# Performance work log

Measured on AMD Instinct MI355X. Metric: run time of the kernel, lower is better.

Reference implementation:

```python
import jax, jax.numpy as jnp
import numpy as np

T_STEP = 0.01
N_STEPS = 1000
H_S = 64
N_TARGETS = 2048
INPUT_S = 2
H_NN = 256
ACTION_S = 2


def setup_inputs() -> dict:
    key = jax.random.key(0)
    ks = jax.random.split(key, 9)
    target = jax.random.normal(ks[0], (N_TARGETS, INPUT_S), dtype=jnp.float32)
    D = jax.random.normal(ks[1], (H_S,), dtype=jnp.float32) * 0.1
    P = jax.random.normal(ks[2], (H_S, H_S), dtype=jnp.float32)
    l1_w = jax.random.normal(ks[3], (H_NN, INPUT_S), dtype=jnp.float32) * 0.05
    l1_b = jax.random.normal(ks[4], (H_NN,), dtype=jnp.float32) * 0.05
    l2_w = jax.random.normal(ks[5], (H_S, H_NN), dtype=jnp.float32) * 0.05
    l2_b = jax.random.normal(ks[6], (H_S,), dtype=jnp.float32) * 0.05
    lm_w = jax.random.normal(ks[7], (ACTION_S, H_S), dtype=jnp.float32) * 0.05
    lm_b = jax.random.normal(ks[8], (ACTION_S,), dtype=jnp.float32) * 0.05
    return {"target": target, "D": D, "P": P,
            "l1_w": l1_w, "l1_b": l1_b, "l2_w": l2_w, "l2_b": l2_b,
            "lm_w": lm_w, "lm_b": lm_b}


def reference(target, D, P, l1_w, l1_b, l2_w, l2_b, lm_w, lm_b):
    # initial condition MLP: relu(l1) -> l2, then transpose to (h_s, n_targets)
    h = jax.nn.relu(target @ l1_w.T + l1_b)           # (n_targets, h_nn)
    x0 = (h @ l2_w.T + l2_b).T                        # (h_s, n_targets)
    # A = P diag(exp(D)) P^-1 ; step map x <- (I - dt*A) x
    A = (P * jnp.exp(D)[None, :]) @ jnp.linalg.inv(P)  # (h_s, h_s)
    M = jnp.eye(H_S, dtype=A.dtype) - T_STEP * A

    def step(x, _):
        act = jnp.tanh(x.T @ lm_w.T + lm_b)            # (n_targets, action_s)
        return M @ x, (x, act)

    _, (hidden_states, acts) = jax.lax.scan(step, x0, None, length=N_STEPS)
    # hidden_states: (n_steps, h_s, n_targets); acts: (n_steps, n_targets, action_s)
    actions = jnp.transpose(acts, (1, 2, 0))           # (n_targets, action_s, n_steps)
    return actions, hidden_states
```

## Files before the change

### kernel.cpp

```cpp
#include <hip/hip_runtime.h>
#include <math.h>

#define NT 2048
#define HS 64
#define HNN 256
#define NSTEPS 1000
#define TSTEP 0.01f

typedef unsigned short u16;
typedef __attribute__((ext_vector_type(8))) short bf16x8;
typedef __attribute__((ext_vector_type(4))) float f32x4;

#define OFF_PINV 0
#define OFF_HT   148736

#define S_H 1028

__device__ inline void bsplit(float x, u16& hi, u16& lo) {
    unsigned u = __float_as_uint(x);
    unsigned r = (u + 0x7FFFu + ((u >> 16) & 1u)) >> 16;
    hi = (u16)r;
    float xh = __uint_as_float(r << 16);
    float d = x - xh;
    unsigned v = __float_as_uint(d);
    unsigned s = (v + 0x7FFFu + ((v >> 16) & 1u)) >> 16;
    lo = (u16)s;
}

__device__ inline void bar_lds() {
    asm volatile("s_waitcnt lgkmcnt(0)" ::: "memory");
    __builtin_amdgcn_s_barrier();
    asm volatile("" ::: "memory");
}

__device__ inline float tanh_fast(float x) {
    float xc = fminf(fmaxf(x, -15.f), 15.f);
    float a = __builtin_amdgcn_exp2f(xc * 2.885390082f);
    return (a - 1.f) * __builtin_amdgcn_rcpf(a + 1.f);
}

__global__ __launch_bounds__(512) void k_gj(const float* __restrict__ P,
                                            float* __restrict__ ws) {
    __shared__ float Aug[64 * 130];
    __shared__ float fvec[2][64];
    int tid = threadIdx.x;

    for (int idx = tid; idx < 64 * 128; idx += 512) {
        int r = idx >> 7, c = idx & 127;
        Aug[r * 130 + c] = (c < 64) ? P[r * 64 + c] : ((c - 64) == r ? 1.f : 0.f);
    }
    __syncthreads();

    if (tid < 64) {
        float nv = Aug[tid * 130];
        float pv = __shfl(nv, 0);
        fvec[0][tid] = (tid == 0) ? 0.f : nv / pv;
    }
    __syncthreads();

    for (int t = 0; t < 64; ++t) {
        int par = t & 1;
        if (tid < 64) {
            int col0 = (t < 63) ? (t + 1) : 64;
            float f = fvec[par][tid];
            float src = Aug[t * 130 + col0];
            float nv = Aug[tid * 130 + col0] - f * src;
            Aug[tid * 130 + col0] = nv;
            if (t < 63) {
                float pv = __shfl(nv, t + 1);
                fvec[par ^ 1][tid] = (tid == (t + 1)) ? 0.f : nv / pv;
            }
        } else {
            int w = (tid >> 6) - 1;
            int lane = tid & 63;
            float f = fvec[par][lane];
            const float* rowp = Aug + t * 130;
            float* rowr = Aug + lane * 130;
            int pcnt = 63 - t;
            for (int s = 1 + w; s < 64; s += 7) {
                int col = (s < pcnt) ? (t + 1 + s) : (64 + (s - pcnt));
                rowr[col] -= f * rowp[col];
            }
        }
        __syncthreads();
    }

    for (int idx = tid; idx < 4096; idx += 512) {
        int j = idx >> 6, m = idx & 63;
        ws[OFF_PINV + j * 64 + m] = Aug[j * 130 + 64 + m] / Aug[j * 130 + j];
    }
}

__global__ __launch_bounds__(512) void k_y0fa(const float* __restrict__ target,
                                              const float* __restrict__ l1_w,
                                              const float* __restrict__ l1_b,
                                              const float* __restrict__ l2_w,
                                              const float* __restrict__ l2_b,
                                              const float* __restrict__ lm_w,
                                              const float* __restrict__ lm_b,
                                              const float* __restrict__ D,
                                              const float* __restrict__ P,
                                              float* __restrict__ ws,
                                              float* __restrict__ actions) {
    int ct = blockIdx.x;
    int cbase = ct * 16;
    int tid = threadIdx.x;
    __shared__ float tgt[16][2];
    __shared__ union { float shT[256 * 17]; float rs[64 * 17]; float us[16][128]; } u;
    __shared__ float x0s[64 * 17];
    __shared__ float y0s[64 * 17];
    __shared__ float lam_s[64], l2l_s[64];
    __shared__ float Q_s[128];

    if (tid < 16) {
        float2 tv = ((const float2*)target)[cbase + tid];
        tgt[tid][0] = tv.x; tgt[tid][1] = tv.y;
    } else if (tid >= 64 && tid < 128) {
        int i = tid - 64;
        float l = 1.0f - TSTEP * expf(D[i]);
        lam_s[i] = l;
        l2l_s[i] = log2f(l);
    } else if (tid >= 128 && tid < 256) {
        int t = tid - 128;
        int a = t >> 6, i = t & 63;
        float s = 0.f;
        for (int r = 0; r < 64; ++r) s = fmaf(lm_w[a * 64 + r], P[r * 64 + i], s);
        Q_s[t] = s;
    }
    __syncthreads();
    if (tid < 256) {
        float w0 = l1_w[2 * tid], w1 = l1_w[2 * tid + 1], bb = l1_b[tid];
        #pragma unroll
        for (int cc = 0; cc < 16; ++cc)
            u.shT[tid * 17 + cc] =
                fmaxf(fmaf(w0, tgt[cc][0], fmaf(w1, tgt[cc][1], bb)), 0.f);
    }
    __syncthreads();
    int i = tid >> 3, cs = (tid & 7) * 2;
    {
        const float* l2wi = l2_w + i * 256;
        float bb = l2_b[i];
        float a0 = bb, a1 = bb;
        #pragma unroll 4
        for (int j = 0; j < 256; ++j) {
            float w = l2wi[j];
            a0 = fmaf(w, u.shT[j * 17 + cs], a0);
            a1 = fmaf(w, u.shT[j * 17 + cs + 1], a1);
        }
        x0s[i * 17 + cs] = a0; x0s[i * 17 + cs + 1] = a1;
    }
    __syncthreads();
    const float* Ri = ws + OFF_PINV + i * 64;
    {
        float b0 = 0, b1 = 0;
        #pragma unroll 4
        for (int m = 0; m < 64; ++m) {
            float rv = Ri[m];
            b0 = fmaf(rv, x0s[m * 17 + cs], b0);
            b1 = fmaf(rv, x0s[m * 17 + cs + 1], b1);
        }
        y0s[i * 17 + cs] = b0; y0s[i * 17 + cs + 1] = b1;
    }
    __syncthreads();
    const float* Pi = P + i * 64;
    #pragma unroll 1
    for (int it = 0; it < 2; ++it) {
        float r0 = x0s[i * 17 + cs], r1 = x0s[i * 17 + cs + 1];
        #pragma unroll 4
        for (int m = 0; m < 64; ++m) {
            float pv = Pi[m];
            r0 = fmaf(-pv, y0s[m * 17 + cs], r0);
            r1 = fmaf(-pv, y0s[m * 17 + cs + 1], r1);
        }
        u.rs[i * 17 + cs] = r0; u.rs[i * 17 + cs + 1] = r1;
        __syncthreads();
        float d0 = 0, d1 = 0;
        #pragma unroll 4
        for (int m = 0; m < 64; ++m) {
            float rv = Ri[m];
            d0 = fmaf(rv, u.rs[m * 17 + cs], d0);
            d1 = fmaf(rv, u.rs[m * 17 + cs + 1], d1);
        }
        y0s[i * 17 + cs] += d0; y0s[i * 17 + cs + 1] += d1;
        __syncthreads();
    }

    for (int idx = tid; idx < 2048; idx += 512) {
        int cgi = idx >> 7, t = idx & 127;
        u.us[cgi][t] = Q_s[t] * y0s[(t & 63) * 17 + cgi];
    }
    if (tid < 128) {
        int kt = tid >> 6, lane = tid & 63;
        int c_l = lane & 15;
        int i0 = kt * 32 + (lane >> 4) * 8;
        u16* YH = (u16*)(ws + OFF_HT);
        u16* YL = YH + 131072;
        bf16x8 vh, vl;
        #pragma unroll
        for (int j = 0; j < 8; ++j) {
            u16 h, lo;
            bsplit(y0s[(i0 + j) * 17 + c_l], h, lo);
            vh[j] = (short)h; vl[j] = (short)lo;
        }
        int off = ((ct * 2 + kt) * 64 + lane);
        *(bf16x8*)(YH + off * 8) = vh;
        *(bf16x8*)(YL + off * 8) = vl;
    }
    __syncthreads();

    if (tid < 500) {
        int k0 = tid * 2;
        float b0 = lm_b[0], b1 = lm_b[1];
        float fk0 = (float)k0;
        #pragma unroll 1
        for (int ch = 0; ch < 4; ++ch) {
            int cg0 = ch * 4;
            float2 s[4][2];
            #pragma unroll
            for (int j = 0; j < 4; ++j) {
                s[j][0] = make_float2(b0, b0);
                s[j][1] = make_float2(b1, b1);
            }
            #pragma unroll 4
            for (int ii = 0; ii < 64; ++ii) {
                float p0 = __builtin_amdgcn_exp2f(fk0 * l2l_s[ii]);
                float p1 = p0 * lam_s[ii];
                #pragma unroll
                for (int j = 0; j < 4; ++j) {
                    float u0 = u.us[cg0 + j][ii];
                    float u1 = u.us[cg0 + j][64 + ii];
                    s[j][0].x = fmaf(u0, p0, s[j][0].x);
                    s[j][0].y = fmaf(u0, p1, s[j][0].y);
                    s[j][1].x = fmaf(u1, p0, s[j][1].x);
                    s[j][1].y = fmaf(u1, p1, s[j][1].y);
                }
            }
            #pragma unroll
            for (int j = 0; j < 4; ++j)
                #pragma unroll
                for (int a = 0; a < 2; ++a) {
                    float2 r;
                    r.x = tanh_fast(s[j][a].x);
                    r.y = tanh_fast(s[j][a].y);
                    *(float2*)(actions + (size_t)(cbase + cg0 + j) * 2000 + a * 1000 + k0) = r;
                }
        }
    }
}

__global__ __launch_bounds__(512, 2) void k_hidden(const float* __restrict__ P,
                                                   const float* __restrict__ D,
                                                   const float* __restrict__ ws,
                                                   float* __restrict__ hidden) {
    int k = blockIdx.x;
    int tid = threadIdx.x;
    int wid = tid >> 6, lane = tid & 63;
    int l15 = lane & 15, lg = lane >> 4;

    extern __shared__ float stage[];
    __shared__ float lp_s[64];

    const u16* YH = (const u16*)(ws + OFF_HT);
    const u16* YL = YH + 131072;

    if (tid < 64) {
        float l = 1.0f - TSTEP * expf(D[tid]);
        lp_s[tid] = exp2f((float)k * log2f(l));
    }
    __syncthreads();

    bf16x8 ah[4][2], al[4][2];
    #pragma unroll
    for (int rt = 0; rt < 4; ++rt) {
        int r = rt * 16 + l15;
        #pragma unroll
        for (int kt = 0; kt < 2; ++kt) {
            int i0 = kt * 32 + lg * 8;
            #pragma unroll
            for (int j = 0; j < 8; ++j) {
                float v = P[r * 64 + i0 + j] * lp_s[i0 + j];
                u16 h, lo;
                bsplit(v, h, lo);
                ah[rt][kt][j] = (short)h;
                al[rt][kt][j] = (short)lo;
            }
        }
    }

    float* outk = hidden + (size_t)k * 64 * NT;

    #pragma unroll 1
    for (int half = 0; half < 2; ++half) {
        bf16x8 bh[8][2], bl[8][2];
        #pragma unroll
        for (int q = 0; q < 8; ++q)
            #pragma unroll
            for (int kt = 0; kt < 2; ++kt) {
                int ct_g = half * 64 + wid * 8 + q;
                int off = ((ct_g * 2 + kt) * 64 + lane) * 8;
                bh[q][kt] = *(const bf16x8*)(YH + off);
                bl[q][kt] = *(const bf16x8*)(YL + off);
            }
        #pragma unroll
        for (int rt = 0; rt < 4; ++rt) {
            #pragma unroll
            for (int q = 0; q < 8; ++q) {
                f32x4 acc = {0.f, 0.f, 0.f, 0.f};
                #pragma unroll
                for (int kt = 0; kt < 2; ++kt) {
                    acc = __builtin_amdgcn_mfma_f32_16x16x32_bf16(ah[rt][kt], bh[q][kt], acc, 0, 0, 0);
                    acc = __builtin_amdgcn_mfma_f32_16x16x32_bf16(al[rt][kt], bh[q][kt], acc, 0, 0, 0);
                    acc = __builtin_amdgcn_mfma_f32_16x16x32_bf16(ah[rt][kt], bl[q][kt], acc, 0, 0, 0);
                }
                int col = wid * 128 + q * 16 + l15;
                #pragma unroll
                for (int reg = 0; reg < 4; ++reg)
                    stage[(lg * 4 + reg) * S_H + col] = acc[reg];
            }
            bar_lds();
            #pragma unroll
            for (int it = 0; it < 8; ++it) {
                int f = it * 512 + tid;
                int r = f >> 8, c4 = f & 255;
                float4 v = *(const float4*)&stage[r * S_H + (c4 << 2)];
                *(float4*)(outk + (size_t)(rt * 16 + r) * NT + half * 1024 + (c4 << 2)) = v;
            }
            bar_lds();
        }
    }
}

extern "C" void kernel_launch(void* const* d_in, const int* in_sizes, int n_in,
                              void* d_out, int out_size, void* d_ws, size_t ws_size,
                              hipStream_t stream) {
    const float* target = (const float*)d_in[0];
    const float* D      = (const float*)d_in[1];
    const float* P      = (const float*)d_in[2];
    const float* l1_w   = (const float*)d_in[3];
    const float* l1_b   = (const float*)d_in[4];
    const float* l2_w   = (const float*)d_in[5];
    const float* l2_b   = (const float*)d_in[6];
    const float* lm_w   = (const float*)d_in[7];
    const float* lm_b   = (const float*)d_in[8];
    float* ws = (float*)d_ws;
    float* actions = (float*)d_out;
    float* hidden  = (float*)d_out + 4096000;

    hipFuncSetAttribute((const void*)k_hidden,
                        hipFuncAttributeMaxDynamicSharedMemorySize, 16 * S_H * 4);

    hipLaunchKernelGGL(k_gj,     dim3(1),    dim3(512), 0, stream, P, ws);
    hipLaunchKernelGGL(k_y0fa,   dim3(128),  dim3(512), 0, stream,
                       target, l1_w, l1_b, l2_w, l2_b, lm_w, lm_b, D, P, ws, actions);
    hipLaunchKernelGGL(k_hidden, dim3(1000), dim3(512), 16 * S_H * 4, stream, P, D, ws, hidden);
}
```

Before: 201.8 us.

## Fuse matrix inverse into front kernel with redundant per-block Gauss-Jordan

```diff
diff --git a/kernel.cpp b/kernel.cpp
--- a/kernel.cpp
+++ b/kernel.cpp
@@ -11,7 +11,6 @@
 typedef __attribute__((ext_vector_type(8))) short bf16x8;
 typedef __attribute__((ext_vector_type(4))) float f32x4;
 
-#define OFF_PINV 0
 #define OFF_HT   148736
 
 #define S_H 1028
@@ -39,11 +38,38 @@
     return (a - 1.f) * __builtin_amdgcn_rcpf(a + 1.f);
 }
 
-__global__ __launch_bounds__(512) void k_gj(const float* __restrict__ P,
-                                            float* __restrict__ ws) {
-    __shared__ float Aug[64 * 130];
-    __shared__ float fvec[2][64];
+struct FrontSh {
+    union {
+        float Aug[64 * 130];
+        struct {
+            union { float shT[256 * 17]; float rs[64 * 17]; float us[16 * 128]; } a;
+            float x0s[64 * 17];
+            float y0s[64 * 17];
+        } p2;
+    } u;
+    float Rs[64 * 65];
+    float fvec[2][64];
+    float tgt[16][2];
+    float lam_s[64], l2l_s[64];
+    float Q_s[128];
+};
+
+__global__ __launch_bounds__(512) void k_front(const float* __restrict__ target,
+                                               const float* __restrict__ l1_w,
+                                               const float* __restrict__ l1_b,
+                                               const float* __restrict__ l2_w,
+                                               const float* __restrict__ l2_b,
+                                               const float* __restrict__ lm_w,
+                                               const float* __restrict__ lm_b,
+                                               const float* __restrict__ D,
+                                               const float* __restrict__ P,
+                                               float* __restrict__ ws,
+                                               float* __restrict__ actions) {
+    __shared__ FrontSh sh;
+    int ct = blockIdx.x;
+    int cbase = ct * 16;
     int tid = threadIdx.x;
+    float* Aug = sh.u.Aug;
 
     for (int idx = tid; idx < 64 * 128; idx += 512) {
         int r = idx >> 7, c = idx & 127;
@@ -54,7 +80,22 @@
     if (tid < 64) {
         float nv = Aug[tid * 130];
         float pv = __shfl(nv, 0);
-        fvec[0][tid] = (tid == 0) ? 0.f : nv / pv;
+        sh.fvec[0][tid] = (tid == 0) ? 0.f : nv * __builtin_amdgcn_rcpf(pv);
+    } else if (tid < 128) {
+        int i = tid - 64;
+        float l = 1.0f - TSTEP * expf(D[i]);
+        sh.lam_s[i] = l;
+        sh.l2l_s[i] = log2f(l);
+    } else if (tid < 256) {
+        int t = tid - 128;
+        int a = t >> 6, i = t & 63;
+        float s = 0.f;
+        for (int r = 0; r < 64; ++r) s = fmaf(lm_w[a * 64 + r], P[r * 64 + i], s);
+        sh.Q_s[t] = s;
+    } else if (tid < 272) {
+        int c = tid - 256;
+        float2 tv = ((const float2*)target)[cbase + c];
+        sh.tgt[c][0] = tv.x; sh.tgt[c][1] = tv.y;
     }
     __syncthreads();
 
@@ -62,18 +103,19 @@
         int par = t & 1;
         if (tid < 64) {
             int col0 = (t < 63) ? (t + 1) : 64;
-            float f = fvec[par][tid];
+            float f = sh.fvec[par][tid];
             float src = Aug[t * 130 + col0];
             float nv = Aug[tid * 130 + col0] - f * src;
             Aug[tid * 130 + col0] = nv;
             if (t < 63) {
                 float pv = __shfl(nv, t + 1);
-                fvec[par ^ 1][tid] = (tid == (t + 1)) ? 0.f : nv / pv;
+                sh.fvec[par ^ 1][tid] = (tid == (t + 1)) ? 0.f
+                                        : nv * __builtin_amdgcn_rcpf(pv);
             }
         } else {
             int w = (tid >> 6) - 1;
             int lane = tid & 63;
-            float f = fvec[par][lane];
+            float f = sh.fvec[par][lane];
             const float* rowp = Aug + t * 130;
             float* rowr = Aug + lane * 130;
             int pcnt = 63 - t;
@@ -87,55 +129,20 @@
 
     for (int idx = tid; idx < 4096; idx += 512) {
         int j = idx >> 6, m = idx & 63;
-        ws[OFF_PINV + j * 64 + m] = Aug[j * 130 + 64 + m] / Aug[j * 130 + j];
-    }
-}
-
-__global__ __launch_bounds__(512) void k_y0fa(const float* __restrict__ target,
-                                              const float* __restrict__ l1_w,
-                                              const float* __restrict__ l1_b,
-                                              const float* __restrict__ l2_w,
-                                              const float* __restrict__ l2_b,
-                                              const float* __restrict__ lm_w,
-                                              const float* __restrict__ lm_b,
-                                              const float* __restrict__ D,
-                                              const float* __restrict__ P,
-                                              float* __restrict__ ws,
-                                              float* __restrict__ actions) {
-    int ct = blockIdx.x;
-    int cbase = ct * 16;
-    int tid = threadIdx.x;
-    __shared__ float tgt[16][2];
-    __shared__ union { float shT[256 * 17]; float rs[64 * 17]; float us[16][128]; } u;
-    __shared__ float x0s[64 * 17];
-    __shared__ float y0s[64 * 17];
-    __shared__ float lam_s[64], l2l_s[64];
-    __shared__ float Q_s[128];
-
-    if (tid < 16) {
-        float2 tv = ((const float2*)target)[cbase + tid];
-        tgt[tid][0] = tv.x; tgt[tid][1] = tv.y;
-    } else if (tid >= 64 && tid < 128) {
-        int i = tid - 64;
-        float l = 1.0f - TSTEP * expf(D[i]);
-        lam_s[i] = l;
-        l2l_s[i] = log2f(l);
-    } else if (tid >= 128 && tid < 256) {
-        int t = tid - 128;
-        int a = t >> 6, i = t & 63;
-        float s = 0.f;
-        for (int r = 0; r < 64; ++r) s = fmaf(lm_w[a * 64 + r], P[r * 64 + i], s);
-        Q_s[t] = s;
-    }
-    __syncthreads();
+        sh.Rs[j * 65 + m] = Aug[j * 130 + 64 + m]
+                            * __builtin_amdgcn_rcpf(Aug[j * 130 + j]);
+    }
+    __syncthreads();
+
     if (tid < 256) {
         float w0 = l1_w[2 * tid], w1 = l1_w[2 * tid + 1], bb = l1_b[tid];
         #pragma unroll
         for (int cc = 0; cc < 16; ++cc)
-            u.shT[tid * 17 + cc] =
-                fmaxf(fmaf(w0, tgt[cc][0], fmaf(w1, tgt[cc][1], bb)), 0.f);
-    }
-    __syncthreads();
+            sh.u.p2.a.shT[tid * 17 + cc] =
+                fmaxf(fmaf(w0, sh.tgt[cc][0], fmaf(w1, sh.tgt[cc][1], bb)), 0.f);
+    }
+    __syncthreads();
+
     int i = tid >> 3, cs = (tid & 7) * 2;
     {
         const float* l2wi = l2_w + i * 256;
@@ -144,50 +151,53 @@
         #pragma unroll 4
         for (int j = 0; j < 256; ++j) {
             float w = l2wi[j];
-            a0 = fmaf(w, u.shT[j * 17 + cs], a0);
-            a1 = fmaf(w, u.shT[j * 17 + cs + 1], a1);
-        }
-        x0s[i * 17 + cs] = a0; x0s[i * 17 + cs + 1] = a1;
-    }
-    __syncthreads();
-    const float* Ri = ws + OFF_PINV + i * 64;
+            a0 = fmaf(w, sh.u.p2.a.shT[j * 17 + cs], a0);
+            a1 = fmaf(w, sh.u.p2.a.shT[j * 17 + cs + 1], a1);
+        }
+        sh.u.p2.x0s[i * 17 + cs] = a0; sh.u.p2.x0s[i * 17 + cs + 1] = a1;
+    }
+    __syncthreads();
+
+    const float* Ri = sh.Rs + i * 65;
     {
         float b0 = 0, b1 = 0;
         #pragma unroll 4
         for (int m = 0; m < 64; ++m) {
             float rv = Ri[m];
-            b0 = fmaf(rv, x0s[m * 17 + cs], b0);
-            b1 = fmaf(rv, x0s[m * 17 + cs + 1], b1);
-        }
-        y0s[i * 17 + cs] = b0; y0s[i * 17 + cs + 1] = b1;
-    }
-    __syncthreads();
+            b0 = fmaf(rv, sh.u.p2.x0s[m * 17 + cs], b0);
+            b1 = fmaf(rv, sh.u.p2.x0s[m * 17 + cs + 1], b1);
+        }
+        sh.u.p2.y0s[i * 17 + cs] = b0; sh.u.p2.y0s[i * 17 + cs + 1] = b1;
+    }
+    __syncthreads();
+
     const float* Pi = P + i * 64;
     #pragma unroll 1
     for (int it = 0; it < 2; ++it) {
-        float r0 = x0s[i * 17 + cs], r1 = x0s[i * 17 + cs + 1];
+        float r0 = sh.u.p2.x0s[i * 17 + cs], r1 = sh.u.p2.x0s[i * 17 + cs + 1];
         #pragma unroll 4
         for (int m = 0; m < 64; ++m) {
             float pv = Pi[m];
-            r0 = fmaf(-pv, y0s[m * 17 + cs], r0);
-            r1 = fmaf(-pv, y0s[m * 17 + cs + 1], r1);
-        }
-        u.rs[i * 17 + cs] = r0; u.rs[i * 17 + cs + 1] = r1;
+            r0 = fmaf(-pv, sh.u.p2.y0s[m * 17 + cs], r0);
+            r1 = fmaf(-pv, sh.u.p2.y0s[m * 17 + cs + 1], r1);
+        }
+        __syncthreads();
+        sh.u.p2.a.rs[i * 17 + cs] = r0; sh.u.p2.a.rs[i * 17 + cs + 1] = r1;
         __syncthreads();
         float d0 = 0, d1 = 0;
         #pragma unroll 4
         for (int m = 0; m < 64; ++m) {
             float rv = Ri[m];
-            d0 = fmaf(rv, u.rs[m * 17 + cs], d0);
-            d1 = fmaf(rv, u.rs[m * 17 + cs + 1], d1);
-        }
-        y0s[i * 17 + cs] += d0; y0s[i * 17 + cs + 1] += d1;
+            d0 = fmaf(rv, sh.u.p2.a.rs[m * 17 + cs], d0);
+            d1 = fmaf(rv, sh.u.p2.a.rs[m * 17 + cs + 1], d1);
+        }
+        sh.u.p2.y0s[i * 17 + cs] += d0; sh.u.p2.y0s[i * 17 + cs + 1] += d1;
         __syncthreads();
     }
 
     for (int idx = tid; idx < 2048; idx += 512) {
         int cgi = idx >> 7, t = idx & 127;
-        u.us[cgi][t] = Q_s[t] * y0s[(t & 63) * 17 + cgi];
+        sh.u.p2.a.us[cgi * 128 + t] = sh.Q_s[t] * sh.u.p2.y0s[(t & 63) * 17 + cgi];
     }
     if (tid < 128) {
         int kt = tid >> 6, lane = tid & 63;
@@ -199,7 +209,7 @@
         #pragma unroll
         for (int j = 0; j < 8; ++j) {
             u16 h, lo;
-            bsplit(y0s[(i0 + j) * 17 + c_l], h, lo);
+            bsplit(sh.u.p2.y0s[(i0 + j) * 17 + c_l], h, lo);
             vh[j] = (short)h; vl[j] = (short)lo;
         }
         int off = ((ct * 2 + kt) * 64 + lane);
@@ -223,12 +233,12 @@
             }
             #pragma unroll 4
             for (int ii = 0; ii < 64; ++ii) {
-                float p0 = __builtin_amdgcn_exp2f(fk0 * l2l_s[ii]);
-                float p1 = p0 * lam_s[ii];
+                float p0 = __builtin_amdgcn_exp2f(fk0 * sh.l2l_s[ii]);
+                float p1 = p0 * sh.lam_s[ii];
                 #pragma unroll
                 for (int j = 0; j < 4; ++j) {
-                    float u0 = u.us[cg0 + j][ii];
-                    float u1 = u.us[cg0 + j][64 + ii];
+                    float u0 = sh.u.p2.a.us[(cg0 + j) * 128 + ii];
+                    float u1 = sh.u.p2.a.us[(cg0 + j) * 128 + 64 + ii];
                     s[j][0].x = fmaf(u0, p0, s[j][0].x);
                     s[j][0].y = fmaf(u0, p1, s[j][0].y);
                     s[j][1].x = fmaf(u1, p0, s[j][1].x);
@@ -349,8 +359,7 @@
     hipFuncSetAttribute((const void*)k_hidden,
                         hipFuncAttributeMaxDynamicSharedMemorySize, 16 * S_H * 4);
 
-    hipLaunchKernelGGL(k_gj,     dim3(1),    dim3(512), 0, stream, P, ws);
-    hipLaunchKernelGGL(k_y0fa,   dim3(128),  dim3(512), 0, stream,
+    hipLaunchKernelGGL(k_front,  dim3(128),  dim3(512), 0, stream,
                        target, l1_w, l1_b, l2_w, l2_b, lm_w, lm_b, D, P, ws, actions);
     hipLaunchKernelGGL(k_hidden, dim3(1000), dim3(512), 16 * S_H * 4, stream, P, D, ws, hidden);
 }
```

Measured after the change: 203.0 us. No clear change (+0.6%).
